# Kernel tuning notes

Hardware: AMD Instinct MI355X
Metric: run time of the kernel (lower is better)

The kernel has to match this reference:

```python
import jax, jax.numpy as jnp
import numpy as np

N_NODES = 100000
N_EDGES = 3200000
N_GRAPHS = 64


def _seg_mean(vals, idx, num_segments):
    s = jax.ops.segment_sum(vals, idx, num_segments=num_segments)
    cnt = jax.ops.segment_sum(jnp.ones((vals.shape[0],), vals.dtype), idx,
                              num_segments=num_segments)
    return s / jnp.maximum(cnt, 1.0)[:, None]


def _gcn_layer(x, edge_index, edge_attr, Wc, bc, Wn):
    # center = lin1(x)
    center = x @ Wc + bc
    row, col = edge_index[0], edge_index[1]  # row = source (j), col = target (i)
    # degree computed over row indices (as in PyG degree(row))
    deg = jax.ops.segment_sum(jnp.ones((row.shape[0],), x.dtype), row,
                              num_segments=x.shape[0])
    deg_inv_sqrt = jnp.where(deg > 0, jax.lax.rsqrt(jnp.maximum(deg, 1.0)), 0.0)
    norm = deg_inv_sqrt[row] * deg_inv_sqrt[col]  # [E]
    # message: lin2(concat(x_j, edge_attr)) * norm
    msg = jnp.concatenate([x[row], edge_attr], axis=1) @ Wn  # [E, out]
    msg = msg * norm[:, None]
    # aggr='mean' at target nodes
    aggr = _seg_mean(msg, col, x.shape[0])
    return center + aggr


def setup_inputs() -> dict:
    key = jax.random.key(0)
    ks = jax.random.split(key, 12)
    x = jax.random.normal(ks[0], (N_NODES, 3), dtype=jnp.float32)
    edge_index = jax.random.randint(ks[1], (2, N_EDGES), 0, N_NODES, dtype=jnp.int64)
    edge_attr = jax.random.normal(ks[2], (N_EDGES, 2), dtype=jnp.float32)
    batch = jnp.sort(jax.random.randint(ks[3], (N_NODES,), 0, N_GRAPHS, dtype=jnp.int64))
    s = 0.2
    params = {
        'Wc1': jax.random.normal(ks[4], (3, 16), jnp.float32) * s,
        'bc1': jnp.zeros((16,), jnp.float32),
        'Wn1': jax.random.normal(ks[5], (5, 16), jnp.float32) * s,   # in+edge = 3+2
        'Wc2': jax.random.normal(ks[6], (16, 16), jnp.float32) * s,
        'bc2': jnp.zeros((16,), jnp.float32),
        'Wn2': jax.random.normal(ks[7], (18, 16), jnp.float32) * s,  # 16+2
        'Wl1': jax.random.normal(ks[8], (16, 16), jnp.float32) * s,
        'bl1': jnp.zeros((16,), jnp.float32),
        'Wl2': jax.random.normal(ks[9], (16, 2), jnp.float32) * s,
        'bl2': jnp.zeros((2,), jnp.float32),
    }
    return dict(x=x, edge_index=edge_index, edge_attr=edge_attr, batch=batch, **params)


def reference(x, edge_index, edge_attr, batch,
              Wc1, bc1, Wn1, Wc2, bc2, Wn2, Wl1, bl1, Wl2, bl2):
    h = _gcn_layer(x, edge_index, edge_attr, Wc1, bc1, Wn1)
    h = jax.nn.relu(h)  # dropout is identity in eval mode
    h = _gcn_layer(h, edge_index, edge_attr, Wc2, bc2, Wn2)
    h = jax.nn.relu(h)
    g = _seg_mean(h, batch, N_GRAPHS)          # global scatter_mean pooling [G,16]
    g = jax.nn.relu(g @ Wl1 + bl1)
    return g @ Wl2 + bl2                        # [G, 2]
```

## Files before the change

### kernel.cpp

```cpp
#include <hip/hip_runtime.h>

constexpr int TPB  = 256;
constexpr int TPBW = 1024;
constexpr int TPBS = 512;
constexpr int BSH  = 7;
constexpr int BKN  = 128;
constexpr int MAXB = 800;
constexpr int CAP  = 4608;
constexpr int SBUF = 4608;
constexpr int ITER = 9;
constexpr int SIT  = 7;
constexpr int SEDG = SIT * TPBW;
constexpr int HWL  = 12800;

__device__ __forceinline__ unsigned short f2bf(float f) {
    unsigned u = __float_as_uint(f);
    u += 0x7FFFu + ((u >> 16) & 1u);
    return (unsigned short)(u >> 16);
}
__device__ __forceinline__ float bflo(unsigned u) {
    return __uint_as_float(u << 16);
}
__device__ __forceinline__ float bfhi(unsigned u) {
    return __uint_as_float(u & 0xFFFF0000u);
}

__global__ __launch_bounds__(TPBW)
void k_stage2(const int* __restrict__ ei, const float2* __restrict__ ea,
              int E, int NBKT, int W,
              int* __restrict__ gcnt, int2* __restrict__ staged,
              unsigned int* __restrict__ partialR) {
    __shared__ unsigned int lh[HWL];
    __shared__ int cl[MAXB], gb[MAXB];
    const int p = blockIdx.x, t = threadIdx.x;
    for (int i = t; i < W; i += TPBW) lh[i] = 0;
    for (int b = t; b < NBKT; b += TPBW) cl[b] = 0;
    __syncthreads();
    const int* colA = ei + E;
    const int s = p * SEDG, send = min(s + SEDG, E);
    int rid[SIT], eap[SIT], bk[SIT], rk[SIT];
#pragma unroll
    for (int k = 0; k < SIT; k++) {
        int e = s + t + k * TPBW;
        bk[k] = -1;
        if (e < send) {
            int r = ei[e], c = colA[e];
            atomicAdd(&lh[r >> 3], 1u << ((r & 7) * 4));
            int b = c >> BSH;
            float2 ev = ea[e];
            rid[k] = (r << BSH) | (c & (BKN - 1));
            eap[k] = (int)((unsigned)f2bf(ev.x) | ((unsigned)f2bf(ev.y) << 16));
            bk[k] = b;
            rk[k] = atomicAdd(&cl[b], 1);
        }
    }
    __syncthreads();
    for (int b = t; b < NBKT; b += TPBW) {
        int c = cl[b];
        gb[b] = c ? atomicAdd(&gcnt[b], c) : 0;
    }
    __syncthreads();
#pragma unroll
    for (int k = 0; k < SIT; k++) {
        if (bk[k] >= 0) {
            int pos = gb[bk[k]] + rk[k];
            if (pos < CAP)
                staged[(size_t)bk[k] * CAP + pos] = make_int2(rid[k], eap[k]);
        }
    }
    for (int w = t; w < W; w += TPBW) partialR[(size_t)p * W + w] = lh[w];
}

__global__ __launch_bounds__(512)
void k_xd(const unsigned int* __restrict__ partialR, int NP, int W, int N,
          const float* __restrict__ x,
          float* __restrict__ dis, float4* __restrict__ xd) {
    __shared__ unsigned int sA[8][64], sB[8][64];
    const int wloc = threadIdx.x & 63, lane = threadIdx.x >> 6;
    const int w = blockIdx.x * 64 + wloc;
    unsigned int accA = 0, accB = 0;
    if (w < W) {
        for (int p = lane; p < NP; p += 8) {
            unsigned int v = partialR[(size_t)p * W + w];
            accA += v & 0x0F0F0F0Fu;
            accB += (v >> 4) & 0x0F0F0F0Fu;
        }
    }
    sA[lane][wloc] = accA;
    sB[lane][wloc] = accB;
    __syncthreads();
    if (lane == 0 && w < W) {
#pragma unroll
        for (int l = 1; l < 8; l++) { accA += sA[l][wloc]; accB += sB[l][wloc]; }
        int d[8];
        d[0] = accA & 255; d[2] = (accA >> 8) & 255;
        d[4] = (accA >> 16) & 255; d[6] = accA >> 24;
        d[1] = accB & 255; d[3] = (accB >> 8) & 255;
        d[5] = (accB >> 16) & 255; d[7] = accB >> 24;
        const int n0 = w * 8;
#pragma unroll
        for (int k = 0; k < 8; k++) {
            int n = n0 + k;
            if (n < N) {
                float dv = d[k] ? rsqrtf((float)d[k]) : 0.f;
                dis[n] = dv;
                xd[n] = make_float4(x[3 * (size_t)n], x[3 * (size_t)n + 1],
                                    x[3 * (size_t)n + 2], dv);
            }
        }
    }
}

__global__ __launch_bounds__(TPBS)
void k_sortA(int2* __restrict__ staged, const int* __restrict__ gcnt,
             const float* __restrict__ dis, const float4* __restrict__ xd, int N,
             const float* __restrict__ Wc, const float* __restrict__ bc,
             const float* __restrict__ Wn,
             unsigned short* __restrict__ hb, float2* __restrict__ eaS,
             int* __restrict__ cnt, int* __restrict__ base, int* __restrict__ segN) {
    __shared__ int sbuf[SBUF];
    __shared__ int lfill[BKN], lexc[BKN], tmp[2][BKN];
    __shared__ float lacx[BKN], lacy[BKN], ldisc[BKN];
    __shared__ float sax[BKN], say[BKN], saz[BKN];
    __shared__ float sWc[48], sbc[16], sWn[80];
    const int b = blockIdx.x, t = threadIdx.x;
    const size_t s0 = (size_t)b * CAP;
    const int c0 = b << BSH;
    int cb = gcnt[b]; if (cb > CAP) cb = CAP;
    if (t < BKN) {
        lfill[t] = 0; lacx[t] = 0.f; lacy[t] = 0.f;
        ldisc[t] = (c0 + t < N) ? dis[c0 + t] : 0.f;
    }
    if (t < 48) sWc[t] = Wc[t];
    if (t >= 64 && t < 80) sbc[t - 64] = bc[t - 64];
    if (t >= 128 && t < 208) sWn[t - 128] = Wn[t - 128];
    __syncthreads();
    int rid[ITER], rk[ITER];
#pragma unroll
    for (int k = 0; k < ITER; k++) {
        int e = t + k * TPBS;
        rk[k] = -1;
        if (e < cb) {
            int2 v = staged[s0 + e];
            int j = v.x & (BKN - 1);
            int r = ((unsigned)v.x) >> BSH;
            float nrm = dis[r] * ldisc[j];
            unsigned eap = (unsigned)v.y;
            rid[k] = v.x;
            rk[k] = atomicAdd(&lfill[j], 1);
            unsafeAtomicAdd(&lacx[j], nrm * bflo(eap));
            unsafeAtomicAdd(&lacy[j], nrm * bfhi(eap));
        }
    }
    __syncthreads();
    int buf = 0;
    if (t < BKN) tmp[0][t] = lfill[t];
    __syncthreads();
    for (int off = 1; off < BKN; off <<= 1) {
        if (t < BKN) {
            int nv = tmp[buf][t] + ((t >= off) ? tmp[buf][t - off] : 0);
            tmp[buf ^ 1][t] = nv;
        }
        __syncthreads();
        buf ^= 1;
    }
    if (t < BKN) lexc[t] = tmp[buf][t] - lfill[t];
    __syncthreads();
#pragma unroll
    for (int k = 0; k < ITER; k++) {
        if (rk[k] >= 0) {
            int j = rid[k] & (BKN - 1);
            int pos = lexc[j] + rk[k];
            if (pos < SBUF) sbuf[pos] = (int)(((unsigned)rid[k]) >> BSH);
        }
    }
    __syncthreads();
    int tot = lexc[BKN - 1] + lfill[BKN - 1];
    if (tot > SBUF) tot = SBUF;
    int* ridS = (int*)staged;
    for (int i = t; i < tot; i += TPBS) ridS[s0 * 2 + i] = sbuf[i];
    if (t == 0) segN[b] = tot;
    if (t < BKN) {
        int nd = c0 + t;
        if (nd < N) { cnt[nd] = lfill[t]; base[nd] = lexc[t]; }
    }
    const int grp = t >> 2, sub = t & 3;
    const int node = c0 + grp;
    float a0 = 0.f, a1 = 0.f, a2 = 0.f;
    {
        int e0 = lexc[grp], dg = lfill[grp];
        if (node < N) {
            for (int e = sub; e < dg; e += 4) {
                int r = sbuf[e0 + e];
                float4 q = xd[r];
                a0 += q.w * q.x;
                a1 += q.w * q.y;
                a2 += q.w * q.z;
            }
        }
    }
    a0 += __shfl_down(a0, 2, 4); a0 += __shfl_down(a0, 1, 4);
    a1 += __shfl_down(a1, 2, 4); a1 += __shfl_down(a1, 1, 4);
    a2 += __shfl_down(a2, 2, 4); a2 += __shfl_down(a2, 1, 4);
    if (sub == 0) { sax[grp] = a0; say[grp] = a1; saz[grp] = a2; }
    __syncthreads();
    if (t < BKN) {
        int nd = c0 + t;
        if (nd < N) {
            float inv = 1.0f / fmaxf((float)lfill[t], 1.0f);
            float4 xq = xd[nd];
            float ldt = xq.w;
            float sc3 = ldt * inv;
            float m[5] = {sax[t] * sc3, say[t] * sc3, saz[t] * sc3,
                          lacx[t] * inv, lacy[t] * inv};
            float xv[3] = {xq.x, xq.y, xq.z};
            float o[16];
#pragma unroll
            for (int k = 0; k < 16; k++) {
                float v = sbc[k];
#pragma unroll
                for (int j = 0; j < 3; j++) v += xv[j] * sWc[j * 16 + k];
#pragma unroll
                for (int j = 0; j < 5; j++) v += m[j] * sWn[j * 16 + k];
                o[k] = fmaxf(v, 0.0f);
            }
            unsigned ov[8];
#pragma unroll
            for (int q = 0; q < 8; q++)
                ov[q] = (unsigned)f2bf(o[2 * q]) | ((unsigned)f2bf(o[2 * q + 1]) << 16);
            uint4* hp = (uint4*)(hb + 16 * (size_t)nd);
            hp[0] = make_uint4(ov[0], ov[1], ov[2], ov[3]);
            hp[1] = make_uint4(ov[4], ov[5], ov[6], ov[7]);
            eaS[nd] = make_float2(lacx[t], lacy[t]);
        }
    }
}

__global__ __launch_bounds__(TPBS)
void k_g2(const int* __restrict__ ridS, const int* __restrict__ cnt,
          const int* __restrict__ base, const int* __restrict__ segN,
          const float* __restrict__ dis, const unsigned short* __restrict__ hb,
          const float2* __restrict__ eaS, const int* __restrict__ batch, int N,
          const float* __restrict__ Wc, const float* __restrict__ bc,
          const float* __restrict__ Wn,
          float* __restrict__ pool, int* __restrict__ poolcnt) {
    __shared__ int sbuf[SBUF];
    __shared__ int lfill[BKN], lexc[BKN];
    __shared__ float smr[BKN][17];
    __shared__ float sWc[256], sbc[16], sWn[288], sp[1024];
    __shared__ int sc[64];
    const int b = blockIdx.x, t = threadIdx.x;
    const size_t s0 = (size_t)b * CAP * 2;
    const int c0 = b << BSH;
    if (t < BKN) {
        int nd = c0 + t;
        lfill[t] = (nd < N) ? cnt[nd] : 0;
        lexc[t]  = (nd < N) ? base[nd] : 0;
    }
    for (int k = t; k < 256; k += TPBS) sWc[k] = Wc[k];
    for (int k = t; k < 16;  k += TPBS) sbc[k] = bc[k];
    for (int k = t; k < 288; k += TPBS) sWn[k] = Wn[k];
    for (int k = t; k < 1024; k += TPBS) sp[k] = 0.f;
    if (t < 64) sc[t] = 0;
    int tot = segN[b];
    if (tot > SBUF) tot = SBUF;
    for (int i = t; i < tot; i += TPBS) sbuf[i] = ridS[s0 + i];
    __syncthreads();
    const int grp = t >> 2, sub = t & 3;
    const int node = c0 + grp;
    float mm[16];
#pragma unroll
    for (int k = 0; k < 16; k++) mm[k] = 0.f;
    if (node < N) {
        int e0 = lexc[grp], dg = lfill[grp];
        for (int e = sub; e < dg; e += 4) {
            int r = sbuf[e0 + e];
            float w = dis[r];
            const uint4* hr = (const uint4*)(hb + 16 * (size_t)r);
            uint4 A = hr[0], B = hr[1];
            mm[0]  += w * bflo(A.x);  mm[1]  += w * bfhi(A.x);
            mm[2]  += w * bflo(A.y);  mm[3]  += w * bfhi(A.y);
            mm[4]  += w * bflo(A.z);  mm[5]  += w * bfhi(A.z);
            mm[6]  += w * bflo(A.w);  mm[7]  += w * bfhi(A.w);
            mm[8]  += w * bflo(B.x);  mm[9]  += w * bfhi(B.x);
            mm[10] += w * bflo(B.y);  mm[11] += w * bfhi(B.y);
            mm[12] += w * bflo(B.z);  mm[13] += w * bfhi(B.z);
            mm[14] += w * bflo(B.w);  mm[15] += w * bfhi(B.w);
        }
    }
#pragma unroll
    for (int k = 0; k < 16; k++) {
        mm[k] += __shfl_down(mm[k], 2, 4);
        mm[k] += __shfl_down(mm[k], 1, 4);
    }
    if (sub == 0) {
#pragma unroll
        for (int k = 0; k < 16; k++) smr[grp][k] = mm[k];
    }
    __syncthreads();
    if (t < BKN) {
        int nd = c0 + t;
        if (nd < N) {
            float inv = 1.0f / fmaxf((float)lfill[t], 1.0f);
            float ldt = dis[nd];
            float scm = ldt * inv;
            float m[18];
#pragma unroll
            for (int k = 0; k < 16; k++) m[k] = smr[t][k] * scm;
            float2 es = eaS[nd];
            m[16] = es.x * inv; m[17] = es.y * inv;
            const uint4* hp = (const uint4*)(hb + 16 * (size_t)nd);
            uint4 A = hp[0], B = hp[1];
            float hv[16] = {bflo(A.x), bfhi(A.x), bflo(A.y), bfhi(A.y),
                            bflo(A.z), bfhi(A.z), bflo(A.w), bfhi(A.w),
                            bflo(B.x), bfhi(B.x), bflo(B.y), bfhi(B.y),
                            bflo(B.z), bfhi(B.z), bflo(B.w), bfhi(B.w)};
            int g = batch[nd];
            atomicAdd(&sc[g], 1);
#pragma unroll
            for (int k = 0; k < 16; k++) {
                float v = sbc[k];
#pragma unroll
                for (int j = 0; j < 16; j++) v += hv[j] * sWc[j * 16 + k];
#pragma unroll
                for (int j = 0; j < 18; j++) v += m[j] * sWn[j * 16 + k];
                v = fmaxf(v, 0.0f);
                unsafeAtomicAdd(&sp[g * 16 + k], v);
            }
        }
    }
    __syncthreads();
    for (int k = t; k < 1024; k += TPBS)
        if (sp[k] != 0.0f) unsafeAtomicAdd(&pool[k], sp[k]);
    if (t < 64 && sc[t]) atomicAdd(&poolcnt[t], sc[t]);
}

__global__ void k_final(const float* __restrict__ pool, const int* __restrict__ poolcnt,
                        const float* __restrict__ Wl1, const float* __restrict__ bl1,
                        const float* __restrict__ Wl2, const float* __restrict__ bl2,
                        float* __restrict__ out) {
    int g = threadIdx.x;
    if (g >= 64) return;
    float inv = 1.0f / fmaxf((float)poolcnt[g], 1.0f);
    float gv[16];
#pragma unroll
    for (int k = 0; k < 16; k++) gv[k] = pool[g * 16 + k] * inv;
    float t[16];
#pragma unroll
    for (int k = 0; k < 16; k++) {
        float v = bl1[k];
#pragma unroll
        for (int j = 0; j < 16; j++) v += gv[j] * Wl1[j * 16 + k];
        t[k] = fmaxf(v, 0.0f);
    }
    float o0 = bl2[0], o1 = bl2[1];
#pragma unroll
    for (int j = 0; j < 16; j++) {
        o0 += t[j] * Wl2[j * 2 + 0];
        o1 += t[j] * Wl2[j * 2 + 1];
    }
    out[2 * g + 0] = o0;
    out[2 * g + 1] = o1;
}

extern "C" void kernel_launch(void* const* d_in, const int* in_sizes, int n_in,
                              void* d_out, int out_size, void* d_ws, size_t ws_size,
                              hipStream_t stream) {
    const float* x     = (const float*)d_in[0];
    const int*   ei    = (const int*)  d_in[1];
    const float* ea    = (const float*)d_in[2];
    const int*   batch = (const int*)  d_in[3];
    const float* Wc1   = (const float*)d_in[4];
    const float* bc1   = (const float*)d_in[5];
    const float* Wn1   = (const float*)d_in[6];
    const float* Wc2   = (const float*)d_in[7];
    const float* bc2   = (const float*)d_in[8];
    const float* Wn2   = (const float*)d_in[9];
    const float* Wl1   = (const float*)d_in[10];
    const float* bl1   = (const float*)d_in[11];
    const float* Wl2   = (const float*)d_in[12];
    const float* bl2   = (const float*)d_in[13];
    float* out = (float*)d_out;

    const int N  = in_sizes[0] / 3;
    const int E  = in_sizes[1] / 2;
    const int NBKT = (N + BKN - 1) >> BSH;
    const int SGRID = (E + SEDG - 1) / SEDG;
    const int W = (N + 7) >> 3;

    char* ws = (char*)d_ws;
    size_t o = 0;
    auto alloc = [&](size_t bytes) {
        void* p = ws + o;
        o += (bytes + 255) & ~(size_t)255;
        return p;
    };
    float* pool    = (float*)alloc(64 * 16 * 4);
    int*   poolcnt = (int*)  alloc(64 * 4);
    int*   gcnt    = (int*)  alloc((size_t)NBKT * 4);
    size_t zbytes = o;
    float*  dis     = (float*)alloc((size_t)N * 4);
    float4* xd      = (float4*)alloc((size_t)N * 16);
    float2* eaS     = (float2*)alloc((size_t)N * 8);
    int*    cnt     = (int*)  alloc((size_t)N * 4);
    int*    base    = (int*)  alloc((size_t)N * 4);
    int*    segN    = (int*)  alloc((size_t)NBKT * 4);
    unsigned int* partialR = (unsigned int*)alloc((size_t)SGRID * W * 4);
    int2*   staged  = (int2*)alloc((size_t)NBKT * CAP * 8);
    unsigned short* hb = (unsigned short*)alloc((size_t)N * 16 * 2);
    (void)ws_size;

    hipMemsetAsync(d_ws, 0, zbytes, stream);

    k_stage2<<<SGRID, TPBW, 0, stream>>>(ei, (const float2*)ea, E, NBKT, W,
                                         gcnt, staged, partialR);
    k_xd    <<<(W + 63) / 64, 512, 0, stream>>>(partialR, SGRID, W, N, x, dis, xd);
    k_sortA <<<NBKT, TPBS, 0, stream>>>(staged, gcnt, dis, xd, N,
                                        Wc1, bc1, Wn1, hb, eaS, cnt, base, segN);
    k_g2    <<<NBKT, TPBS, 0, stream>>>((const int*)staged, cnt, base, segN,
                                        dis, hb, eaS, batch, N,
                                        Wc2, bc2, Wn2, pool, poolcnt);
    k_final <<<1, 64, 0, stream>>>(pool, poolcnt, Wl1, bl1, Wl2, bl2, out);
}
```

Baseline: 284.1 us.

## Prescale layer-1 features by source degree and move edge-attr sums into sorted gather

Layer one now writes a second bf16 copy of each node's hidden features already multiplied by its source inverse-sqrt degree. This lets layer two's gather sum the rows directly without loading dis[r] per edge. The edge-attribute aggregation moves from shared-memory float atomics during bucketing into the per-node gather loop over a sorted int2 buffer, and the 128-entry block scan is replaced by a wavefront shuffle scan. The cost is an extra N×16 bf16 buffer write, an int2 shared buffer twice the previous size, and a changed rounding order since the product is now rounded to bf16 before summation.

```diff
diff --git a/kernel.cpp b/kernel.cpp
--- a/kernel.cpp
+++ b/kernel.cpp
@@ -113,29 +113,27 @@
 
 __global__ __launch_bounds__(TPBS)
 void k_sortA(int2* __restrict__ staged, const int* __restrict__ gcnt,
-             const float* __restrict__ dis, const float4* __restrict__ xd, int N,
+             const float4* __restrict__ xd, int N,
              const float* __restrict__ Wc, const float* __restrict__ bc,
              const float* __restrict__ Wn,
-             unsigned short* __restrict__ hb, float2* __restrict__ eaS,
+             unsigned short* __restrict__ hb, unsigned short* __restrict__ hbs,
+             float2* __restrict__ eaS,
              int* __restrict__ cnt, int* __restrict__ base, int* __restrict__ segN) {
-    __shared__ int sbuf[SBUF];
-    __shared__ int lfill[BKN], lexc[BKN], tmp[2][BKN];
-    __shared__ float lacx[BKN], lacy[BKN], ldisc[BKN];
-    __shared__ float sax[BKN], say[BKN], saz[BKN];
+    __shared__ int2 sbuf2[SBUF];
+    __shared__ int lfill[BKN], lexc[BKN];
+    __shared__ float sax[BKN], say[BKN], saz[BKN], se1[BKN], se2[BKN];
     __shared__ float sWc[48], sbc[16], sWn[80];
+    __shared__ int stot;
     const int b = blockIdx.x, t = threadIdx.x;
     const size_t s0 = (size_t)b * CAP;
     const int c0 = b << BSH;
     int cb = gcnt[b]; if (cb > CAP) cb = CAP;
-    if (t < BKN) {
-        lfill[t] = 0; lacx[t] = 0.f; lacy[t] = 0.f;
-        ldisc[t] = (c0 + t < N) ? dis[c0 + t] : 0.f;
-    }
+    if (t < BKN) lfill[t] = 0;
     if (t < 48) sWc[t] = Wc[t];
     if (t >= 64 && t < 80) sbc[t - 64] = bc[t - 64];
     if (t >= 128 && t < 208) sWn[t - 128] = Wn[t - 128];
     __syncthreads();
-    int rid[ITER], rk[ITER];
+    int er[ITER], ep[ITER], rk[ITER];
 #pragma unroll
     for (int k = 0; k < ITER; k++) {
         int e = t + k * TPBS;
@@ -143,66 +141,70 @@
         if (e < cb) {
             int2 v = staged[s0 + e];
             int j = v.x & (BKN - 1);
-            int r = ((unsigned)v.x) >> BSH;
-            float nrm = dis[r] * ldisc[j];
-            unsigned eap = (unsigned)v.y;
-            rid[k] = v.x;
-            rk[k] = atomicAdd(&lfill[j], 1);
-            unsafeAtomicAdd(&lacx[j], nrm * bflo(eap));
-            unsafeAtomicAdd(&lacy[j], nrm * bfhi(eap));
-        }
-    }
-    __syncthreads();
-    int buf = 0;
-    if (t < BKN) tmp[0][t] = lfill[t];
-    __syncthreads();
-    for (int off = 1; off < BKN; off <<= 1) {
-        if (t < BKN) {
-            int nv = tmp[buf][t] + ((t >= off) ? tmp[buf][t - off] : 0);
-            tmp[buf ^ 1][t] = nv;
-        }
-        __syncthreads();
-        buf ^= 1;
-    }
-    if (t < BKN) lexc[t] = tmp[buf][t] - lfill[t];
+            er[k] = (int)(((unsigned)v.x) >> BSH);
+            ep[k] = v.y;
+            rk[k] = atomicAdd(&lfill[j], 1) | (j << 16);
+        }
+    }
+    __syncthreads();
+    if (t < 64) {
+        int v0 = lfill[2 * t], v1 = lfill[2 * t + 1];
+        int sv = v0 + v1, incl = sv;
+#pragma unroll
+        for (int off = 1; off < 64; off <<= 1) {
+            int up = __shfl_up(incl, off, 64);
+            if (t >= off) incl += up;
+        }
+        int exc = incl - sv;
+        lexc[2 * t]     = exc;
+        lexc[2 * t + 1] = exc + v0;
+        if (t == 63) stot = incl;
+    }
     __syncthreads();
 #pragma unroll
     for (int k = 0; k < ITER; k++) {
         if (rk[k] >= 0) {
-            int j = rid[k] & (BKN - 1);
-            int pos = lexc[j] + rk[k];
-            if (pos < SBUF) sbuf[pos] = (int)(((unsigned)rid[k]) >> BSH);
-        }
-    }
-    __syncthreads();
-    int tot = lexc[BKN - 1] + lfill[BKN - 1];
-    if (tot > SBUF) tot = SBUF;
-    int* ridS = (int*)staged;
-    for (int i = t; i < tot; i += TPBS) ridS[s0 * 2 + i] = sbuf[i];
+            int j = rk[k] >> 16, rr = rk[k] & 0xFFFF;
+            sbuf2[lexc[j] + rr] = make_int2(er[k], ep[k]);
+        }
+    }
+    __syncthreads();
+    int tot = stot; if (tot > SBUF) tot = SBUF;
+    const int grp = t >> 2, sub = t & 3;
+    const int node = c0 + grp;
+    float a0 = 0.f, a1 = 0.f, a2 = 0.f, b1 = 0.f, b2 = 0.f;
+    {
+        int e0 = lexc[grp], dg = lfill[grp];
+        if (node < N) {
+            for (int e = sub; e < dg; e += 4) {
+                int2 ve = sbuf2[e0 + e];
+                float4 q = xd[ve.x];
+                a0 += q.w * q.x;
+                a1 += q.w * q.y;
+                a2 += q.w * q.z;
+                b1 += q.w * bflo((unsigned)ve.y);
+                b2 += q.w * bfhi((unsigned)ve.y);
+            }
+        }
+    }
+    a0 += __shfl_down(a0, 2, 4); a0 += __shfl_down(a0, 1, 4);
+    a1 += __shfl_down(a1, 2, 4); a1 += __shfl_down(a1, 1, 4);
+    a2 += __shfl_down(a2, 2, 4); a2 += __shfl_down(a2, 1, 4);
+    b1 += __shfl_down(b1, 2, 4); b1 += __shfl_down(b1, 1, 4);
+    b2 += __shfl_down(b2, 2, 4); b2 += __shfl_down(b2, 1, 4);
+    if (sub == 0) {
+        sax[grp] = a0; say[grp] = a1; saz[grp] = a2;
+        se1[grp] = b1; se2[grp] = b2;
+    }
+    {
+        int* ridS = (int*)staged;
+        for (int i = t; i < tot; i += TPBS) ridS[s0 * 2 + i] = sbuf2[i].x;
+    }
     if (t == 0) segN[b] = tot;
     if (t < BKN) {
         int nd = c0 + t;
         if (nd < N) { cnt[nd] = lfill[t]; base[nd] = lexc[t]; }
     }
-    const int grp = t >> 2, sub = t & 3;
-    const int node = c0 + grp;
-    float a0 = 0.f, a1 = 0.f, a2 = 0.f;
-    {
-        int e0 = lexc[grp], dg = lfill[grp];
-        if (node < N) {
-            for (int e = sub; e < dg; e += 4) {
-                int r = sbuf[e0 + e];
-                float4 q = xd[r];
-                a0 += q.w * q.x;
-                a1 += q.w * q.y;
-                a2 += q.w * q.z;
-            }
-        }
-    }
-    a0 += __shfl_down(a0, 2, 4); a0 += __shfl_down(a0, 1, 4);
-    a1 += __shfl_down(a1, 2, 4); a1 += __shfl_down(a1, 1, 4);
-    a2 += __shfl_down(a2, 2, 4); a2 += __shfl_down(a2, 1, 4);
-    if (sub == 0) { sax[grp] = a0; say[grp] = a1; saz[grp] = a2; }
     __syncthreads();
     if (t < BKN) {
         int nd = c0 + t;
@@ -210,9 +212,9 @@
             float inv = 1.0f / fmaxf((float)lfill[t], 1.0f);
             float4 xq = xd[nd];
             float ldt = xq.w;
-            float sc3 = ldt * inv;
-            float m[5] = {sax[t] * sc3, say[t] * sc3, saz[t] * sc3,
-                          lacx[t] * inv, lacy[t] * inv};
+            float sc = ldt * inv;
+            float m[5] = {sax[t] * sc, say[t] * sc, saz[t] * sc,
+                          se1[t] * sc, se2[t] * sc};
             float xv[3] = {xq.x, xq.y, xq.z};
             float o[16];
 #pragma unroll
@@ -224,14 +226,20 @@
                 for (int j = 0; j < 5; j++) v += m[j] * sWn[j * 16 + k];
                 o[k] = fmaxf(v, 0.0f);
             }
-            unsigned ov[8];
-#pragma unroll
-            for (int q = 0; q < 8; q++)
+            unsigned ov[8], sv[8];
+#pragma unroll
+            for (int q = 0; q < 8; q++) {
                 ov[q] = (unsigned)f2bf(o[2 * q]) | ((unsigned)f2bf(o[2 * q + 1]) << 16);
+                sv[q] = (unsigned)f2bf(ldt * o[2 * q]) |
+                        ((unsigned)f2bf(ldt * o[2 * q + 1]) << 16);
+            }
             uint4* hp = (uint4*)(hb + 16 * (size_t)nd);
             hp[0] = make_uint4(ov[0], ov[1], ov[2], ov[3]);
             hp[1] = make_uint4(ov[4], ov[5], ov[6], ov[7]);
-            eaS[nd] = make_float2(lacx[t], lacy[t]);
+            uint4* hps = (uint4*)(hbs + 16 * (size_t)nd);
+            hps[0] = make_uint4(sv[0], sv[1], sv[2], sv[3]);
+            hps[1] = make_uint4(sv[4], sv[5], sv[6], sv[7]);
+            eaS[nd] = make_float2(se1[t] * ldt, se2[t] * ldt);
         }
     }
 }
@@ -240,6 +248,7 @@
 void k_g2(const int* __restrict__ ridS, const int* __restrict__ cnt,
           const int* __restrict__ base, const int* __restrict__ segN,
           const float* __restrict__ dis, const unsigned short* __restrict__ hb,
+          const unsigned short* __restrict__ hbs,
           const float2* __restrict__ eaS, const int* __restrict__ batch, int N,
           const float* __restrict__ Wc, const float* __restrict__ bc,
           const float* __restrict__ Wn,
@@ -275,17 +284,16 @@
         int e0 = lexc[grp], dg = lfill[grp];
         for (int e = sub; e < dg; e += 4) {
             int r = sbuf[e0 + e];
-            float w = dis[r];
-            const uint4* hr = (const uint4*)(hb + 16 * (size_t)r);
+            const uint4* hr = (const uint4*)(hbs + 16 * (size_t)r);
             uint4 A = hr[0], B = hr[1];
-            mm[0]  += w * bflo(A.x);  mm[1]  += w * bfhi(A.x);
-            mm[2]  += w * bflo(A.y);  mm[3]  += w * bfhi(A.y);
-            mm[4]  += w * bflo(A.z);  mm[5]  += w * bfhi(A.z);
-            mm[6]  += w * bflo(A.w);  mm[7]  += w * bfhi(A.w);
-            mm[8]  += w * bflo(B.x);  mm[9]  += w * bfhi(B.x);
-            mm[10] += w * bflo(B.y);  mm[11] += w * bfhi(B.y);
-            mm[12] += w * bflo(B.z);  mm[13] += w * bfhi(B.z);
-            mm[14] += w * bflo(B.w);  mm[15] += w * bfhi(B.w);
+            mm[0]  += bflo(A.x);  mm[1]  += bfhi(A.x);
+            mm[2]  += bflo(A.y);  mm[3]  += bfhi(A.y);
+            mm[4]  += bflo(A.z);  mm[5]  += bfhi(A.z);
+            mm[6]  += bflo(A.w);  mm[7]  += bfhi(A.w);
+            mm[8]  += bflo(B.x);  mm[9]  += bfhi(B.x);
+            mm[10] += bflo(B.y);  mm[11] += bfhi(B.y);
+            mm[12] += bflo(B.z);  mm[13] += bfhi(B.z);
+            mm[14] += bflo(B.w);  mm[15] += bfhi(B.w);
         }
     }
 #pragma unroll
@@ -407,7 +415,8 @@
     int*    segN    = (int*)  alloc((size_t)NBKT * 4);
     unsigned int* partialR = (unsigned int*)alloc((size_t)SGRID * W * 4);
     int2*   staged  = (int2*)alloc((size_t)NBKT * CAP * 8);
-    unsigned short* hb = (unsigned short*)alloc((size_t)N * 16 * 2);
+    unsigned short* hb  = (unsigned short*)alloc((size_t)N * 16 * 2);
+    unsigned short* hbs = (unsigned short*)alloc((size_t)N * 16 * 2);
     (void)ws_size;
 
     hipMemsetAsync(d_ws, 0, zbytes, stream);
@@ -415,10 +424,11 @@
     k_stage2<<<SGRID, TPBW, 0, stream>>>(ei, (const float2*)ea, E, NBKT, W,
                                          gcnt, staged, partialR);
     k_xd    <<<(W + 63) / 64, 512, 0, stream>>>(partialR, SGRID, W, N, x, dis, xd);
-    k_sortA <<<NBKT, TPBS, 0, stream>>>(staged, gcnt, dis, xd, N,
-                                        Wc1, bc1, Wn1, hb, eaS, cnt, base, segN);
+    k_sortA <<<NBKT, TPBS, 0, stream>>>(staged, gcnt, xd, N,
+                                        Wc1, bc1, Wn1, hb, hbs, eaS,
+                                        cnt, base, segN);
     k_g2    <<<NBKT, TPBS, 0, stream>>>((const int*)staged, cnt, base, segN,
-                                        dis, hb, eaS, batch, N,
+                                        dis, hb, hbs, eaS, batch, N,
                                         Wc2, bc2, Wn2, pool, poolcnt);
     k_final <<<1, 64, 0, stream>>>(pool, poolcnt, Wl1, bl1, Wl2, bl2, out);
 }
```

Result: faster. 247.1 us (-13.0%).
